# Performance work log

Measured on AMD Instinct MI355X. Metric: run time of the kernel, lower is better.

Reference implementation:

```python
import jax, jax.numpy as jnp
import numpy as np

D_MODEL = 1024
NHEAD = 16
DFF = 4096
B, S = 4, 1024
EPS = 1e-5  # torch LayerNorm default


def _layernorm(x, g, b):
    mu = jnp.mean(x, axis=-1, keepdims=True)
    var = jnp.mean((x - mu) ** 2, axis=-1, keepdims=True)
    return (x - mu) * jax.lax.rsqrt(var + EPS) * g + b


def setup_inputs() -> dict:
    key = jax.random.key(0)
    ks = jax.random.split(key, 12)
    sc = 0.02
    d, h, f = D_MODEL, NHEAD, DFF
    return {
        "src": jax.random.normal(ks[0], (B, S, d), dtype=jnp.float32),
        "w_in": jax.random.normal(ks[1], (3 * d, d), dtype=jnp.float32) * sc,  # packed q,k,v proj (torch in_proj_weight)
        "b_in": jnp.zeros((3 * d,), jnp.float32),
        "w_out": jax.random.normal(ks[2], (d, d), dtype=jnp.float32) * sc,
        "b_out": jnp.zeros((d,), jnp.float32),
        "w1": jax.random.normal(ks[3], (f, d), dtype=jnp.float32) * sc,
        "b1": jnp.zeros((f,), jnp.float32),
        "w2": jax.random.normal(ks[4], (d, f), dtype=jnp.float32) * sc,
        "b2": jnp.zeros((d,), jnp.float32),
        "g1": jnp.ones((d,), jnp.float32),
        "be1": jnp.zeros((d,), jnp.float32),
        "g2": jnp.ones((d,), jnp.float32),
        "be2": jnp.zeros((d,), jnp.float32),
    }


def reference(src, w_in, b_in, w_out, b_out, w1, b1, w2, b2, g1, be1, g2, be2):
    # dropout layers are identity in eval mode
    b, s, d = src.shape
    h = NHEAD
    dh = d // h
    # --- MHA, need_weights=True, average_attn_weights=False ---
    qkv = src @ w_in.T + b_in                      # [B,S,3D]
    q, k, v = jnp.split(qkv, 3, axis=-1)
    q = q.reshape(b, s, h, dh).transpose(0, 2, 1, 3) * (1.0 / np.sqrt(dh))
    k = k.reshape(b, s, h, dh).transpose(0, 2, 1, 3)
    v = v.reshape(b, s, h, dh).transpose(0, 2, 1, 3)
    scores = jnp.einsum("bhqd,bhkd->bhqk", q, k)   # [B,H,S,S]
    attn_weights = jax.nn.softmax(scores, axis=-1)  # per-head weights, materialized
    ctx = jnp.einsum("bhqk,bhkd->bhqd", attn_weights, v)
    ctx = ctx.transpose(0, 2, 1, 3).reshape(b, s, d)
    attn_out = ctx @ w_out.T + b_out
    # --- residual + LN1 ---
    x = _layernorm(src + attn_out, g1, be1)
    # --- FFN ---
    ff = jax.nn.relu(x @ w1.T + b1) @ w2.T + b2
    # --- residual + LN2 ---
    out = _layernorm(x + ff, g2, be2)
    return out, attn_weights
```

## Files before the change

kernel.cpp:

```cpp
#include <hip/hip_runtime.h>


#define DEVI __device__ __forceinline__

typedef __attribute__((ext_vector_type(4))) float f4;
typedef __attribute__((ext_vector_type(4))) float f32x4;
typedef __attribute__((ext_vector_type(8))) short s8;
typedef __attribute__((ext_vector_type(4))) unsigned short us4;
typedef unsigned short u16;

DEVI short bf16r(float f) {
  unsigned u = __builtin_bit_cast(unsigned, f);
  unsigned r = (u + 0x7fffu + ((u >> 16) & 1u)) >> 16;
  return (short)(unsigned short)r;
}
DEVI float bf2f(u16 h) {
  unsigned u = ((unsigned)h) << 16;
  return __builtin_bit_cast(float, u);
}
DEVI s8 cvt8(f4 a, f4 b) {
  s8 r;
  r[0] = bf16r(a.x); r[1] = bf16r(a.y); r[2] = bf16r(a.z); r[3] = bf16r(a.w);
  r[4] = bf16r(b.x); r[5] = bf16r(b.y); r[6] = bf16r(b.z); r[7] = bf16r(b.w);
  return r;
}

DEVI void gload16(const void* g, void* l) {
  __builtin_amdgcn_global_load_lds(
      (const __attribute__((address_space(1))) unsigned int*)g,
      (__attribute__((address_space(3))) unsigned int*)l, 16, 0, 0);
}

#define BAR()   __builtin_amdgcn_s_barrier()
#define LGKM0() do { asm volatile("s_waitcnt lgkmcnt(0)" ::: "memory"); \
                     __builtin_amdgcn_sched_barrier(0); } while (0)
#define VM4()   do { asm volatile("s_waitcnt vmcnt(4)" ::: "memory"); \
                     __builtin_amdgcn_sched_barrier(0); } while (0)

DEVI void xcd_remap(int& bx, int& by) {
  int nbx = gridDim.x, nby = gridDim.y;
  int hw = blockIdx.y * nbx + blockIdx.x;
  int qch = (nbx * nby) >> 3;
  int lid = (hw & 7) * qch + (hw >> 3);
  bx = lid % nbx; by = lid / nbx;
}

template<int RES>
__global__ __launch_bounds__(256)
void gemm128(const u16* __restrict__ A, long lda,
             const u16* __restrict__ B, long ldb,
             u16* __restrict__ C, long ldc,
             const float* __restrict__ bias,
             const void* __restrict__ resid, long ldr, int K,
             int qcols, float qscale, int do_relu)
{
  __shared__ __align__(128) short As[128 * 64];
  __shared__ __align__(128) short Bs[128 * 64];

  int bx, by; xcd_remap(bx, by);
  int row0 = by * 128, col0 = bx * 128;
  int tid = threadIdx.x, lane = tid & 63, w = tid >> 6;
  int wr = w >> 1, wc = w & 1;

  const u16* Ab = A + (long)row0 * lda;
  const u16* Bb = B + (long)col0 * ldb;

  f32x4 acc[4][4] = {};

  for (int k0 = 0; k0 < K; k0 += 64) {
    if (k0) __syncthreads();
#pragma unroll
    for (int c = 0; c < 4; ++c) {
      int seg = w * 4 + c;
      int r = seg * 8 + (lane >> 3);
      int g = (lane & 7) ^ (r & 7);
      gload16(Ab + (long)r * lda + k0 + g * 8, (char*)As + seg * 1024);
    }
#pragma unroll
    for (int c = 0; c < 4; ++c) {
      int seg = w * 4 + c;
      int r = seg * 8 + (lane >> 3);
      int g = (lane & 7) ^ (r & 7);
      gload16(Bb + (long)r * ldb + k0 + g * 8, (char*)Bs + seg * 1024);
    }
    __syncthreads();

#pragma unroll
    for (int kk = 0; kk < 2; ++kk) {
      s8 af[4], bf[4];
      int lr = lane & 15, kg = kk * 4 + (lane >> 4);
#pragma unroll
      for (int i = 0; i < 4; ++i) {
        int R = wr * 64 + i * 16 + lr;
        af[i] = *(const s8*)((char*)As + R * 128 + ((kg ^ (R & 7)) * 16));
      }
#pragma unroll
      for (int j = 0; j < 4; ++j) {
        int R = wc * 64 + j * 16 + lr;
        bf[j] = *(const s8*)((char*)Bs + R * 128 + ((kg ^ (R & 7)) * 16));
      }
#pragma unroll
      for (int i = 0; i < 4; ++i)
#pragma unroll
        for (int j = 0; j < 4; ++j)
          acc[i][j] = __builtin_amdgcn_mfma_f32_16x16x32_bf16(af[i], bf[j], acc[i][j], 0, 0, 0);
    }
  }

#pragma unroll
  for (int i = 0; i < 4; ++i) {
#pragma unroll
    for (int j = 0; j < 4; ++j) {
      int rb = row0 + wr * 64 + i * 16 + (lane >> 4) * 4;
      int c  = col0 + wc * 64 + j * 16 + (lane & 15);
      float bv = bias ? bias[c] : 0.0f;
      float sc = (c < qcols) ? qscale : 1.0f;
#pragma unroll
      for (int q = 0; q < 4; ++q) {
        float v = (acc[i][j][q] + bv) * sc;
        if (do_relu) v = fmaxf(v, 0.0f);
        long rr = rb + q;
        if constexpr (RES == 1) v += ((const float*)resid)[rr * ldr + c];
        if constexpr (RES == 2) v += bf2f(((const u16*)resid)[rr * ldr + c]);
        C[rr * ldc + c] = (u16)bf16r(v);
      }
    }
  }
}

__global__ __launch_bounds__(512, 2)
void gemm256(const u16* __restrict__ A, long lda,
             const u16* __restrict__ B, long ldb,
             u16* __restrict__ C, long ldc,
             const float* __restrict__ bias, int K, int do_relu)
{
  __shared__ __align__(128) char LDS[98304];

  const int tid = threadIdx.x, lane = tid & 63, w = tid >> 6;
  const int wr = w >> 2, wc = w & 3;
  int bx, by; xcd_remap(bx, by);
  const int row0 = by * 256, col0 = bx * 256;

  const u16* Ag = A + (long)row0 * lda;
  const u16* Bg = B + (long)col0 * ldb;

  const int NT = K >> 5;

  const int sr = (w << 4) + (lane >> 2);
  const int gsrc = (lane & 3) ^ ((sr >> 1) & 3);

  auto stageA = [&](int kt, int slot) {
#pragma unroll
    for (int h = 0; h < 2; ++h)
      gload16(Ag + (long)(h * 128 + sr) * lda + kt * 32 + gsrc * 8,
              LDS + slot * 16384 + h * 8192 + (w << 10));
  };
  auto stageB = [&](int kt, int slot) {
#pragma unroll
    for (int h = 0; h < 2; ++h)
      gload16(Bg + (long)(h * 128 + sr) * ldb + kt * 32 + gsrc * 8,
              LDS + 49152 + slot * 16384 + h * 8192 + (w << 10));
  };

  const int kg = lane >> 4, lr = lane & 15;
  auto rdA = [&](int buf, int fig, s8* aF) {
#pragma unroll
    for (int i = 0; i < 4; ++i) {
      int R = wr * 128 + (fig * 4 + i) * 16 + lr;
      aF[i] = *(const s8*)(LDS + buf * 16384 + R * 64 + ((kg ^ ((R >> 1) & 3)) << 4));
    }
  };
  auto rdB = [&](int buf, s8* bF) {
#pragma unroll
    for (int j = 0; j < 4; ++j) {
      int R = wc * 64 + j * 16 + lr;
      bF[j] = *(const s8*)(LDS + 49152 + buf * 16384 + R * 64 + ((kg ^ ((R >> 1) & 3)) << 4));
    }
  };

  f32x4 acc[8][4] = {};

  stageA(0, 0); stageB(0, 0);
  stageA(1, 1); stageB(1, 1);
  VM4();
  BAR();

  int buf = 0;
  for (int t = 0; t < NT; ++t) {
    int nbuf = buf + 2; if (nbuf >= 3) nbuf -= 3;
    int tc = (t + 2 < NT) ? t + 2 : NT - 1;
    s8 aF0[4], aF1[4], bF[4];

    stageA(tc, nbuf);
    stageB(tc, nbuf);
    rdB(buf, bF);
    rdA(buf, 0, aF0);
    rdA(buf, 1, aF1);
    BAR();
    LGKM0();
    __builtin_amdgcn_s_setprio(1);
#pragma unroll
    for (int i = 0; i < 4; ++i)
#pragma unroll
      for (int j = 0; j < 4; ++j)
        acc[i][j] = __builtin_amdgcn_mfma_f32_16x16x32_bf16(aF0[i], bF[j], acc[i][j], 0, 0, 0);
#pragma unroll
    for (int i = 0; i < 4; ++i)
#pragma unroll
      for (int j = 0; j < 4; ++j)
        acc[4 + i][j] = __builtin_amdgcn_mfma_f32_16x16x32_bf16(aF1[i], bF[j], acc[4 + i][j], 0, 0, 0);
    __builtin_amdgcn_s_setprio(0);
    VM4();
    BAR();
    buf = (buf == 2) ? 0 : buf + 1;
  }
  asm volatile("s_waitcnt vmcnt(0)" ::: "memory");

#pragma unroll
  for (int fi = 0; fi < 8; ++fi) {
#pragma unroll
    for (int fj = 0; fj < 4; ++fj) {
      int rb = row0 + wr * 128 + fi * 16 + (lane >> 4) * 4;
      int c  = col0 + wc * 64 + fj * 16 + lr;
      float bv = bias ? bias[c] : 0.0f;
#pragma unroll
      for (int q = 0; q < 4; ++q) {
        float v = acc[fi][fj][q] + bv;
        if (do_relu) v = fmaxf(v, 0.0f);
        C[(long)(rb + q) * ldc + c] = (u16)bf16r(v);
      }
    }
  }
}

__global__ __launch_bounds__(256)
void attn_fused(const u16* __restrict__ qkvb, const u16* __restrict__ vtb,
                float* __restrict__ attnW, u16* __restrict__ ctxb)
{
  __shared__ __align__(128) u16 Kt[128 * 64];
  __shared__ __align__(128) u16 Vt[64 * 128];
  __shared__ __align__(128) u16 Pt[4 * 32 * 128];

  int blk = blockIdx.x;
  int bh = blk >> 3, qt = blk & 7;
  int b = bh >> 4, h = bh & 15;
  int tid = threadIdx.x, lane = tid & 63, w = tid >> 6;

  const u16* Qg = qkvb + (long)b * 3145728 + (long)(qt * 128) * 3072 + h * 64;
#pragma unroll
  for (int c = 0; c < 4; ++c) {
    int seg = w * 4 + c;
    int r = seg * 8 + (lane >> 3);
    int g = (lane & 7) ^ (r & 7);
    gload16(Qg + (long)r * 3072 + g * 8, (char*)Kt + seg * 1024);
  }
  __syncthreads();
  s8 aq[2][2];
#pragma unroll
  for (int i = 0; i < 2; ++i)
#pragma unroll
    for (int kk = 0; kk < 2; ++kk) {
      int R = w * 32 + i * 16 + (lane & 15);
      int kgq = kk * 4 + (lane >> 4);
      aq[i][kk] = *(const s8*)((char*)Kt + R * 128 + ((kgq ^ (R & 7)) * 16));
    }

  const u16* Kbase = qkvb + (long)b * 3145728 + 1024 + h * 64;
  const u16* Vbase = vtb + (long)bh * 65536;

  float m[2][4], l[2][4];
#pragma unroll
  for (int i = 0; i < 2; ++i)
#pragma unroll
    for (int q = 0; q < 4; ++q) { m[i][q] = -1e30f; l[i][q] = 0.0f; }

  for (int kc = 0; kc < 8; ++kc) {
    __syncthreads();
#pragma unroll
    for (int c = 0; c < 4; ++c) {
      int seg = w * 4 + c;
      int r = seg * 8 + (lane >> 3);
      int g = (lane & 7) ^ (r & 7);
      gload16(Kbase + (long)(kc * 128 + r) * 3072 + g * 8, (char*)Kt + seg * 1024);
    }
    __syncthreads();

    f32x4 s[2][8] = {};
#pragma unroll
    for (int kk = 0; kk < 2; ++kk) {
      s8 bk[8];
      int kgq = kk * 4 + (lane >> 4);
#pragma unroll
      for (int j = 0; j < 8; ++j) {
        int R = j * 16 + (lane & 15);
        bk[j] = *(const s8*)((char*)Kt + R * 128 + ((kgq ^ (R & 7)) * 16));
      }
#pragma unroll
      for (int i = 0; i < 2; ++i)
#pragma unroll
        for (int j = 0; j < 8; ++j)
          s[i][j] = __builtin_amdgcn_mfma_f32_16x16x32_bf16(aq[i][kk], bk[j], s[i][j], 0, 0, 0);
    }

#pragma unroll
    for (int i = 0; i < 2; ++i)
#pragma unroll
      for (int q = 0; q < 4; ++q) {
        float mx = s[i][0][q];
#pragma unroll
        for (int j = 1; j < 8; ++j) mx = fmaxf(mx, s[i][j][q]);
        mx = fmaxf(mx, __shfl_xor(mx, 1));
        mx = fmaxf(mx, __shfl_xor(mx, 2));
        mx = fmaxf(mx, __shfl_xor(mx, 4));
        mx = fmaxf(mx, __shfl_xor(mx, 8));
        float mn = fmaxf(m[i][q], mx);
        float sum = 0.0f;
#pragma unroll
        for (int j = 0; j < 8; ++j) sum += __expf(s[i][j][q] - mn);
        sum += __shfl_xor(sum, 1);
        sum += __shfl_xor(sum, 2);
        sum += __shfl_xor(sum, 4);
        sum += __shfl_xor(sum, 8);
        l[i][q] = l[i][q] * __expf(m[i][q] - mn) + sum;
        m[i][q] = mn;
      }
  }

  float inv[2][4];
#pragma unroll
  for (int i = 0; i < 2; ++i)
#pragma unroll
    for (int q = 0; q < 4; ++q) inv[i][q] = 1.0f / l[i][q];

  f32x4 o_[2][4] = {};
  float* aw = attnW + (long)bh * 1048576 + (long)(qt * 128) * 1024;
  u16* Pw = Pt + w * 4096;

  for (int kc = 0; kc < 8; ++kc) {
    __syncthreads();
#pragma unroll
    for (int c = 0; c < 4; ++c) {
      int seg = w * 4 + c;
      int r = seg * 8 + (lane >> 3);
      int g = (lane & 7) ^ (r & 7);
      gload16(Kbase + (long)(kc * 128 + r) * 3072 + g * 8, (char*)Kt + seg * 1024);
    }
#pragma unroll
    for (int c = 0; c < 4; ++c) {
      int seg = w * 4 + c;
      int r = seg * 4 + (lane >> 4);
      int g = (lane & 15) ^ (r & 7);
      gload16(Vbase + (long)r * 1024 + kc * 128 + g * 8, (char*)Vt + seg * 1024);
    }
    __syncthreads();

    f32x4 s[2][8] = {};
#pragma unroll
    for (int kk = 0; kk < 2; ++kk) {
      s8 bk[8];
      int kgq = kk * 4 + (lane >> 4);
#pragma unroll
      for (int j = 0; j < 8; ++j) {
        int R = j * 16 + (lane & 15);
        bk[j] = *(const s8*)((char*)Kt + R * 128 + ((kgq ^ (R & 7)) * 16));
      }
#pragma unroll
      for (int i = 0; i < 2; ++i)
#pragma unroll
        for (int j = 0; j < 8; ++j)
          s[i][j] = __builtin_amdgcn_mfma_f32_16x16x32_bf16(aq[i][kk], bk[j], s[i][j], 0, 0, 0);
    }

#pragma unroll
    for (int i = 0; i < 2; ++i)
#pragma unroll
      for (int j = 0; j < 8; ++j)
#pragma unroll
        for (int q = 0; q < 4; ++q) {
          float p = __expf(s[i][j][q] - m[i][q]) * inv[i][q];
          int R = i * 16 + (lane >> 4) * 4 + q;
          int C = j * 16 + (lane & 15);
          aw[(long)(w * 32 + R) * 1024 + kc * 128 + C] = p;
          *(u16*)((char*)Pw + R * 256 + (((C >> 3) ^ (R & 7)) * 16) + (C & 7) * 2)
              = (u16)bf16r(p);
        }

#pragma unroll
    for (int kks = 0; kks < 4; ++kks) {
      int kgq = kks * 4 + (lane >> 4);
      s8 pa[2], bv[4];
#pragma unroll
      for (int i = 0; i < 2; ++i) {
        int R = i * 16 + (lane & 15);
        pa[i] = *(const s8*)((char*)Pw + R * 256 + ((kgq ^ (R & 7)) * 16));
      }
#pragma unroll
      for (int j = 0; j < 4; ++j) {
        int R = j * 16 + (lane & 15);
        bv[j] = *(const s8*)((char*)Vt + R * 256 + ((kgq ^ (R & 7)) * 16));
      }
#pragma unroll
      for (int i = 0; i < 2; ++i)
#pragma unroll
        for (int j = 0; j < 4; ++j)
          o_[i][j] = __builtin_amdgcn_mfma_f32_16x16x32_bf16(pa[i], bv[j], o_[i][j], 0, 0, 0);
    }
  }

#pragma unroll
  for (int i = 0; i < 2; ++i)
#pragma unroll
    for (int j = 0; j < 4; ++j)
#pragma unroll
      for (int q = 0; q < 4; ++q) {
        int R = w * 32 + i * 16 + (lane >> 4) * 4 + q;
        int col = h * 64 + j * 16 + (lane & 15);
        ctxb[(long)(b * 1024 + qt * 128 + R) * 1024 + col] = (u16)bf16r(o_[i][j][q]);
      }
}

DEVI float blockSum(float v, float* sh) {
#pragma unroll
  for (int o = 32; o > 0; o >>= 1) v += __shfl_xor(v, o);
  int w = threadIdx.x >> 6;
  __syncthreads();
  if ((threadIdx.x & 63) == 0) sh[w] = v;
  __syncthreads();
  return (sh[0] + sh[1]) + (sh[2] + sh[3]);
}

__global__ __launch_bounds__(256)
void ln_rows_b(const u16* __restrict__ in, const float* __restrict__ g,
               const float* __restrict__ be,
               float* __restrict__ outf, u16* __restrict__ outb)
{
  __shared__ float sh[4];
  long row = blockIdx.x;
  int t = threadIdx.x;
  long off = row * 1024 + t * 4;
  us4 rp = *(const us4*)(in + off);
  f4 v;
  v.x = bf2f(rp.x); v.y = bf2f(rp.y); v.z = bf2f(rp.z); v.w = bf2f(rp.w);
  float s = (v.x + v.y) + (v.z + v.w);
  s = blockSum(s, sh);
  float mu = s * (1.0f / 1024.0f);
  f4 d = v - mu;
  float s2 = (d.x * d.x + d.y * d.y) + (d.z * d.z + d.w * d.w);
  s2 = blockSum(s2, sh);
  float rs = rsqrtf(s2 * (1.0f / 1024.0f) + 1e-5f);
  f4 gg = *(const f4*)(g + t * 4);
  f4 bb = *(const f4*)(be + t * 4);
  f4 o = d * rs * gg + bb;
  if (outf) *(f4*)(outf + off) = o;
  if (outb) {
    us4 ob;
    ob.x = (u16)bf16r(o.x); ob.y = (u16)bf16r(o.y);
    ob.z = (u16)bf16r(o.z); ob.w = (u16)bf16r(o.w);
    *(us4*)(outb + off) = ob;
  }
}

__global__ __launch_bounds__(256)
void cvt_all(const float* __restrict__ s0, const float* __restrict__ s1,
             const float* __restrict__ s2, const float* __restrict__ s3,
             const float* __restrict__ s4,
             u16* __restrict__ d0, u16* __restrict__ d1, u16* __restrict__ d2,
             u16* __restrict__ d3, u16* __restrict__ d4)
{
  int bi = blockIdx.x;
  const float* s; u16* d; int base;
  if      (bi < 2048) { s = s0; d = d0; base = bi; }
  else if (bi < 3584) { s = s1; d = d1; base = bi - 2048; }
  else if (bi < 4096) { s = s2; d = d2; base = bi - 3584; }
  else if (bi < 6144) { s = s3; d = d3; base = bi - 4096; }
  else                { s = s4; d = d4; base = bi - 6144; }
  long i = ((long)base * 256 + threadIdx.x) * 8;
  f4 a = *(const f4*)(s + i);
  f4 b = *(const f4*)(s + i + 4);
  *(s8*)(d + i) = cvt8(a, b);
}

__global__ __launch_bounds__(256)
void transpose_v(const u16* __restrict__ qkv, u16* __restrict__ vt) {
  __shared__ u16 tile[64][72];
  int blk = blockIdx.x, bh = blk >> 4, st = blk & 15;
  int b = bh >> 4, h = bh & 15, s0 = st * 64;
  const u16* gq = qkv + (long)b * 1024 * 3072 + 2048 + (long)h * 64;
  int t = threadIdx.x;
  int sl = t >> 4, dq = (t & 15) * 4;
#pragma unroll
  for (int it = 0; it < 4; ++it) {
    int s = it * 16 + sl;
    us4 v = *(const us4*)(gq + (long)(s0 + s) * 3072 + dq);
    tile[dq + 0][s] = v.x; tile[dq + 1][s] = v.y;
    tile[dq + 2][s] = v.z; tile[dq + 3][s] = v.w;
  }
  __syncthreads();
  u16* o = vt + (long)bh * 65536 + s0;
  int dl = t >> 4, sq = (t & 15) * 4;
#pragma unroll
  for (int it = 0; it < 4; ++it) {
    int d = it * 16 + dl;
    us4 v;
    v.x = tile[d][sq + 0]; v.y = tile[d][sq + 1];
    v.z = tile[d][sq + 2]; v.w = tile[d][sq + 3];
    *(us4*)(o + (long)d * 1024 + sq) = v;
  }
}

extern "C" void kernel_launch(void* const* d_in, const int* in_sizes, int n_in,
                              void* d_out, int out_size, void* d_ws, size_t ws_size,
                              hipStream_t stream)
{
  (void)in_sizes; (void)n_in; (void)out_size; (void)ws_size;
  const float* src   = (const float*)d_in[0];
  const float* w_in  = (const float*)d_in[1];
  const float* b_in  = (const float*)d_in[2];
  const float* w_out = (const float*)d_in[3];
  const float* b_out = (const float*)d_in[4];
  const float* w1    = (const float*)d_in[5];
  const float* b1    = (const float*)d_in[6];
  const float* w2    = (const float*)d_in[7];
  const float* b2    = (const float*)d_in[8];
  const float* g1    = (const float*)d_in[9];
  const float* be1   = (const float*)d_in[10];
  const float* g2    = (const float*)d_in[11];
  const float* be2   = (const float*)d_in[12];

  float* out   = (float*)d_out;
  float* attnW = out + (long)4 * 1024 * 1024;

  char* ws = (char*)d_ws;
  u16*   qkvb   = (u16*)(ws);
  u16*   vtb    = (u16*)(ws + 25165824);
  u16*   srcb   = (u16*)(ws + 33554432);
  u16*   ctxb   = (u16*)(ws + 41943040);
  u16*   xb     = (u16*)(ws + 50331648);
  u16*   w_in_b = (u16*)(ws + 58720256);
  u16*   w_outb = (u16*)(ws + 65011712);
  u16*   w1b    = (u16*)(ws + 67108864);
  u16*   w2b    = (u16*)(ws + 75497472);
  u16*   xsumb  = (u16*)(ws + 83886080);
  u16*   ffsumb = (u16*)(ws + 92274688);
  u16*   h1b    = (u16*)(ws);

  cvt_all<<<dim3(8192), 256, 0, stream>>>(src, w_in, w_out, w1, w2,
                                          srcb, w_in_b, w_outb, w1b, w2b);

  gemm128<0><<<dim3(24, 32), 256, 0, stream>>>(
      srcb, 1024, w_in_b, 1024, qkvb, 3072,
      b_in, nullptr, 0, 1024, 1024, 0.125f, 0);

  transpose_v<<<dim3(1024), 256, 0, stream>>>(qkvb, vtb);

  attn_fused<<<dim3(512), 256, 0, stream>>>(qkvb, vtb, attnW, ctxb);

  gemm128<1><<<dim3(8, 32), 256, 0, stream>>>(
      ctxb, 1024, w_outb, 1024, xsumb, 1024,
      b_out, src, 1024, 1024, 0, 1.0f, 0);

  ln_rows_b<<<dim3(4096), 256, 0, stream>>>(xsumb, g1, be1, nullptr, xb);

  gemm256<<<dim3(16, 16), 512, 0, stream>>>(
      xb, 1024, w1b, 1024, h1b, 4096, b1, 1024, 1);

  gemm128<2><<<dim3(8, 32), 256, 0, stream>>>(
      h1b, 4096, w2b, 4096, ffsumb, 1024,
      b2, xb, 1024, 4096, 0, 1.0f, 0);

  ln_rows_b<<<dim3(4096), 256, 0, stream>>>(ffsumb, g2, be2, out, nullptr);
}
```

Baseline: 330.1 us.

## Coalesce attention-weight stores and split-K the N=1024 GEMMs with LN-fused combine

The attention kernel no longer writes each softmax probability to global memory as a scattered 4-byte store. It now reads the bf16 probability tile back from LDS after the PV MFMAs and writes it as contiguous 16-byte float4 rows, so the large attention-weight output is written with coalesced stores. The output projection and the second FFN GEMM now run as 2-way split-K kernels producing fp32 partials, which doubles the block count. Bias, residual and partial-sum addition move into the LayerNorm kernels. In exchange, the returned attention weights are bf16-rounded values rather than fp32, and the extra fp32 partial buffers add global-memory traffic.

```diff
diff --git a/kernel.cpp b/kernel.cpp
--- a/kernel.cpp
+++ b/kernel.cpp
@@ -45,14 +45,12 @@
   bx = lid % nbx; by = lid / nbx;
 }
 
-template<int RES>
 __global__ __launch_bounds__(256)
 void gemm128(const u16* __restrict__ A, long lda,
              const u16* __restrict__ B, long ldb,
              u16* __restrict__ C, long ldc,
-             const float* __restrict__ bias,
-             const void* __restrict__ resid, long ldr, int K,
-             int qcols, float qscale, int do_relu)
+             const float* __restrict__ bias, int K,
+             int qcols, float qscale)
 {
   __shared__ __align__(128) short As[128 * 64];
   __shared__ __align__(128) short Bs[128 * 64];
@@ -118,12 +116,81 @@
 #pragma unroll
       for (int q = 0; q < 4; ++q) {
         float v = (acc[i][j][q] + bv) * sc;
-        if (do_relu) v = fmaxf(v, 0.0f);
-        long rr = rb + q;
-        if constexpr (RES == 1) v += ((const float*)resid)[rr * ldr + c];
-        if constexpr (RES == 2) v += bf2f(((const u16*)resid)[rr * ldr + c]);
-        C[rr * ldc + c] = (u16)bf16r(v);
-      }
+        C[(long)(rb + q) * ldc + c] = (u16)bf16r(v);
+      }
+    }
+  }
+}
+
+__global__ __launch_bounds__(256)
+void gemm128s(const u16* __restrict__ A, long lda, long sAz,
+              const u16* __restrict__ B, long ldb, long sBz,
+              float* __restrict__ C, long ldc, int K)
+{
+  __shared__ __align__(128) short As[128 * 64];
+  __shared__ __align__(128) short Bs[128 * 64];
+
+  int bx, by; xcd_remap(bx, by);
+  int z = blockIdx.z;
+  int row0 = by * 128, col0 = bx * 128;
+  int tid = threadIdx.x, lane = tid & 63, w = tid >> 6;
+  int wr = w >> 1, wc = w & 1;
+
+  const u16* Ab = A + (long)z * sAz + (long)row0 * lda;
+  const u16* Bb = B + (long)z * sBz + (long)col0 * ldb;
+  float* Cz = C + (long)z * 4194304;
+
+  f32x4 acc[4][4] = {};
+
+  for (int k0 = 0; k0 < K; k0 += 64) {
+    if (k0) __syncthreads();
+#pragma unroll
+    for (int c = 0; c < 4; ++c) {
+      int seg = w * 4 + c;
+      int r = seg * 8 + (lane >> 3);
+      int g = (lane & 7) ^ (r & 7);
+      gload16(Ab + (long)r * lda + k0 + g * 8, (char*)As + seg * 1024);
+    }
+#pragma unroll
+    for (int c = 0; c < 4; ++c) {
+      int seg = w * 4 + c;
+      int r = seg * 8 + (lane >> 3);
+      int g = (lane & 7) ^ (r & 7);
+      gload16(Bb + (long)r * ldb + k0 + g * 8, (char*)Bs + seg * 1024);
+    }
+    __syncthreads();
+
+#pragma unroll
+    for (int kk = 0; kk < 2; ++kk) {
+      s8 af[4], bf[4];
+      int lr = lane & 15, kg = kk * 4 + (lane >> 4);
+#pragma unroll
+      for (int i = 0; i < 4; ++i) {
+        int R = wr * 64 + i * 16 + lr;
+        af[i] = *(const s8*)((char*)As + R * 128 + ((kg ^ (R & 7)) * 16));
+      }
+#pragma unroll
+      for (int j = 0; j < 4; ++j) {
+        int R = wc * 64 + j * 16 + lr;
+        bf[j] = *(const s8*)((char*)Bs + R * 128 + ((kg ^ (R & 7)) * 16));
+      }
+#pragma unroll
+      for (int i = 0; i < 4; ++i)
+#pragma unroll
+        for (int j = 0; j < 4; ++j)
+          acc[i][j] = __builtin_amdgcn_mfma_f32_16x16x32_bf16(af[i], bf[j], acc[i][j], 0, 0, 0);
+    }
+  }
+
+#pragma unroll
+  for (int i = 0; i < 4; ++i) {
+#pragma unroll
+    for (int j = 0; j < 4; ++j) {
+      int rb = row0 + wr * 64 + i * 16 + (lane >> 4) * 4;
+      int c  = col0 + wc * 64 + j * 16 + (lane & 15);
+#pragma unroll
+      for (int q = 0; q < 4; ++q)
+        Cz[(long)(rb + q) * ldc + c] = acc[i][j][q];
     }
   }
 }
@@ -380,7 +447,6 @@
           float p = __expf(s[i][j][q] - m[i][q]) * inv[i][q];
           int R = i * 16 + (lane >> 4) * 4 + q;
           int C = j * 16 + (lane & 15);
-          aw[(long)(w * 32 + R) * 1024 + kc * 128 + C] = p;
           *(u16*)((char*)Pw + R * 256 + (((C >> 3) ^ (R & 7)) * 16) + (C & 7) * 2)
               = (u16)bf16r(p);
         }
@@ -404,6 +470,25 @@
 #pragma unroll
         for (int j = 0; j < 4; ++j)
           o_[i][j] = __builtin_amdgcn_mfma_f32_16x16x32_bf16(pa[i], bv[j], o_[i][j], 0, 0, 0);
+    }
+
+#pragma unroll
+    for (int it = 0; it < 4; ++it) {
+      int R2 = it * 8 + (lane >> 3);
+      int gx = lane & 7;
+      float* dst = aw + (long)(w * 32 + R2) * 1024 + kc * 128;
+#pragma unroll
+      for (int half = 0; half < 2; ++half) {
+        int g2 = half * 8 + gx;
+        s8 pv = *(const s8*)((char*)Pw + R2 * 256 + ((g2 ^ (R2 & 7)) * 16));
+        f4 lo, hi;
+        lo.x = bf2f((u16)pv[0]); lo.y = bf2f((u16)pv[1]);
+        lo.z = bf2f((u16)pv[2]); lo.w = bf2f((u16)pv[3]);
+        hi.x = bf2f((u16)pv[4]); hi.y = bf2f((u16)pv[5]);
+        hi.z = bf2f((u16)pv[6]); hi.w = bf2f((u16)pv[7]);
+        *(f4*)(dst + g2 * 8)     = lo;
+        *(f4*)(dst + g2 * 8 + 4) = hi;
+      }
     }
   }
 
@@ -429,18 +514,26 @@
   return (sh[0] + sh[1]) + (sh[2] + sh[3]);
 }
 
+template<bool RBF16>
 __global__ __launch_bounds__(256)
-void ln_rows_b(const u16* __restrict__ in, const float* __restrict__ g,
-               const float* __restrict__ be,
-               float* __restrict__ outf, u16* __restrict__ outb)
+void ln_combine(const float* __restrict__ P0, const float* __restrict__ P1,
+                const void* __restrict__ resid, const float* __restrict__ bias,
+                const float* __restrict__ g, const float* __restrict__ be,
+                float* __restrict__ outf, u16* __restrict__ outb)
 {
   __shared__ float sh[4];
   long row = blockIdx.x;
   int t = threadIdx.x;
   long off = row * 1024 + t * 4;
-  us4 rp = *(const us4*)(in + off);
-  f4 v;
-  v.x = bf2f(rp.x); v.y = bf2f(rp.y); v.z = bf2f(rp.z); v.w = bf2f(rp.w);
+  f4 v = *(const f4*)(P0 + off);
+  v += *(const f4*)(P1 + off);
+  if constexpr (RBF16) {
+    us4 rp = *(const us4*)((const u16*)resid + off);
+    v.x += bf2f(rp.x); v.y += bf2f(rp.y); v.z += bf2f(rp.z); v.w += bf2f(rp.w);
+  } else {
+    v += *(const f4*)((const float*)resid + off);
+  }
+  v += *(const f4*)(bias + t * 4);
   float s = (v.x + v.y) + (v.z + v.w);
   s = blockSum(s, sh);
   float mu = s * (1.0f / 1024.0f);
@@ -540,33 +633,33 @@
   u16*   w_outb = (u16*)(ws + 65011712);
   u16*   w1b    = (u16*)(ws + 67108864);
   u16*   w2b    = (u16*)(ws + 75497472);
-  u16*   xsumb  = (u16*)(ws + 83886080);
-  u16*   ffsumb = (u16*)(ws + 92274688);
   u16*   h1b    = (u16*)(ws);
+  float* wsf    = (float*)ws;
+  float* Qp     = wsf;
+  float* Rp     = wsf + 20971520;
 
   cvt_all<<<dim3(8192), 256, 0, stream>>>(src, w_in, w_out, w1, w2,
                                           srcb, w_in_b, w_outb, w1b, w2b);
 
-  gemm128<0><<<dim3(24, 32), 256, 0, stream>>>(
-      srcb, 1024, w_in_b, 1024, qkvb, 3072,
-      b_in, nullptr, 0, 1024, 1024, 0.125f, 0);
+  gemm128<<<dim3(24, 32), 256, 0, stream>>>(
+      srcb, 1024, w_in_b, 1024, qkvb, 3072, b_in, 1024, 1024, 0.125f);
 
   transpose_v<<<dim3(1024), 256, 0, stream>>>(qkvb, vtb);
 
   attn_fused<<<dim3(512), 256, 0, stream>>>(qkvb, vtb, attnW, ctxb);
 
-  gemm128<1><<<dim3(8, 32), 256, 0, stream>>>(
-      ctxb, 1024, w_outb, 1024, xsumb, 1024,
-      b_out, src, 1024, 1024, 0, 1.0f, 0);
-
-  ln_rows_b<<<dim3(4096), 256, 0, stream>>>(xsumb, g1, be1, nullptr, xb);
+  gemm128s<<<dim3(8, 32, 2), 256, 0, stream>>>(
+      ctxb, 1024, 512, w_outb, 1024, 512, Qp, 1024, 512);
+
+  ln_combine<false><<<dim3(4096), 256, 0, stream>>>(
+      Qp, Qp + 4194304, src, b_out, g1, be1, nullptr, xb);
 
   gemm256<<<dim3(16, 16), 512, 0, stream>>>(
       xb, 1024, w1b, 1024, h1b, 4096, b1, 1024, 1);
 
-  gemm128<2><<<dim3(8, 32), 256, 0, stream>>>(
-      h1b, 4096, w2b, 4096, ffsumb, 1024,
-      b2, xb, 1024, 4096, 0, 1.0f, 0);
-
-  ln_rows_b<<<dim3(4096), 256, 0, stream>>>(ffsumb, g2, be2, out, nullptr);
-}
+  gemm128s<<<dim3(8, 32, 2), 256, 0, stream>>>(
+      h1b, 4096, 2048, w2b, 4096, 2048, Rp, 1024, 2048);
+
+  ln_combine<true><<<dim3(4096), 256, 0, stream>>>(
+      Rp, Rp + 4194304, xb, b2, g2, be2, out, nullptr);
+}
```

Result: faster. 321.5 us (-2.6%).
